# Kernel tuning notes

Measured on AMD Instinct MI355X. Metric: run time of the kernel, lower is better.

The kernel has to match this reference:

```python
import jax, jax.numpy as jnp
import numpy as np

B, S, H = 2, 2048, 2048
N_HEADS, N_KV = 16, 4
HEAD_DIM = H // N_HEADS  # 128
ROPE_THETA = 10000.0


def _rope_tables(seq_len, dim, theta):
    inv_freq = 1.0 / (theta ** (jnp.arange(0, dim, 2, dtype=jnp.float32) / dim))
    t = jnp.arange(seq_len, dtype=jnp.float32)
    freqs = jnp.outer(t, inv_freq)                 # [S, dim/2]
    emb = jnp.concatenate([freqs, freqs], axis=-1)  # [S, dim]
    return jnp.cos(emb), jnp.sin(emb)


def _rotate_half(x):
    x1, x2 = jnp.split(x, 2, axis=-1)
    return jnp.concatenate([-x2, x1], axis=-1)


def setup_inputs() -> dict:
    key = jax.random.key(0)
    ks = jax.random.split(key, 8)
    sc = 0.02
    return {
        "hidden_states": jax.random.normal(ks[0], (B, S, H), jnp.float32),
        "Wq": jax.random.normal(ks[1], (H, N_HEADS * HEAD_DIM), jnp.float32) * sc,
        "bq": jax.random.normal(ks[2], (N_HEADS * HEAD_DIM,), jnp.float32) * sc,
        "Wk": jax.random.normal(ks[3], (H, N_KV * HEAD_DIM), jnp.float32) * sc,
        "bk": jax.random.normal(ks[4], (N_KV * HEAD_DIM,), jnp.float32) * sc,
        "Wv": jax.random.normal(ks[5], (H, N_KV * HEAD_DIM), jnp.float32) * sc,
        "bv": jax.random.normal(ks[6], (N_KV * HEAD_DIM,), jnp.float32) * sc,
        "Wo": jax.random.normal(ks[7], (N_HEADS * HEAD_DIM, H), jnp.float32) * sc,
    }


def reference(hidden_states, Wq, bq, Wk, bk, Wv, bv, Wo):
    bsz, q_len, _ = hidden_states.shape
    q = hidden_states @ Wq + bq  # [B,S,nH*D]
    k = hidden_states @ Wk + bk  # [B,S,nKV*D]
    v = hidden_states @ Wv + bv
    q = q.reshape(bsz, q_len, N_HEADS, HEAD_DIM).transpose(0, 2, 1, 3)   # [B,nH,S,D]
    k = k.reshape(bsz, q_len, N_KV, HEAD_DIM).transpose(0, 2, 1, 3)      # [B,nKV,S,D]
    v = v.reshape(bsz, q_len, N_KV, HEAD_DIM).transpose(0, 2, 1, 3)

    cos, sin = _rope_tables(q_len, HEAD_DIM, ROPE_THETA)  # [S,D]
    cos = cos[None, None].astype(q.dtype)  # [1,1,S,D]
    sin = sin[None, None].astype(q.dtype)
    q = q * cos + _rotate_half(q) * sin
    k = k * cos + _rotate_half(k) * sin

    groups = N_HEADS // N_KV
    k_rep = jnp.repeat(k, groups, axis=1)  # [B,nH,S,D]
    v_rep = jnp.repeat(v, groups, axis=1)

    scale = 1.0 / np.sqrt(HEAD_DIM)
    scores = jnp.einsum("bhqd,bhkd->bhqk", q, k_rep) * scale
    attn = jax.nn.softmax(scores.astype(jnp.float32), axis=-1).astype(q.dtype)
    out = jnp.einsum("bhqk,bhkd->bhqd", attn, v_rep)
    out = out.transpose(0, 2, 1, 3).reshape(bsz, q_len, N_HEADS * HEAD_DIM)
    return out @ Wo
```

## Files before the change

kernel.cpp:

```cpp
#include <hip/hip_runtime.h>
#include <stdint.h>
#include <math.h>

typedef unsigned int u32;
typedef __bf16 bf16x8 __attribute__((ext_vector_type(8)));
typedef float  f32x4  __attribute__((ext_vector_type(4)));
typedef float  f32x16 __attribute__((ext_vector_type(16)));
typedef unsigned int u32x4 __attribute__((ext_vector_type(4)));
typedef unsigned short u16x4 __attribute__((ext_vector_type(4)));
typedef unsigned short u16x8 __attribute__((ext_vector_type(8)));

#define DEV __device__ __forceinline__

DEV unsigned short f2b(float f) {
  u32 x = __builtin_bit_cast(u32, f);
  u32 r = (x + 0x7fffu + ((x >> 16) & 1u)) >> 16;
  return (unsigned short)r;
}
DEV float b2f(unsigned short u) { return __builtin_bit_cast(float, ((u32)u) << 16); }

DEV u32 cvtpk_bf16(float lo, float hi) {
  u32 r;
  asm("v_cvt_pk_bf16_f32 %0, %1, %2" : "=v"(r) : "v"(lo), "v"(hi));
  return r;
}
DEV void pl32swap(u32& a, u32& b) {
  asm("v_permlane32_swap_b32 %0, %1" : "+v"(a), "+v"(b));
}

DEV void gl2lds16(const void* g, void* l) {
  __builtin_amdgcn_global_load_lds((const __attribute__((address_space(1))) u32*)g,
                                   (__attribute__((address_space(3))) u32*)l, 16, 0, 0);
}


__global__ void rope_tables_k(float* __restrict__ ct, float* __restrict__ st) {
  int s = blockIdx.x;
  int d = threadIdx.x;
  float inv = powf(10000.0f, -(float)d / 64.0f);
  float a = (float)s * inv;
  ct[s * 64 + d] = cosf(a);
  st[s * 64 + d] = sinf(a);
}

__global__ void packX_k(const float* __restrict__ in, unsigned short* __restrict__ out,
                        int Mtot) {
  int i = blockIdx.x * blockDim.x + threadIdx.x;
  int k8 = i & 255;
  int m = i >> 8;
  if (m >= Mtot) return;
  const float4* p = (const float4*)(in + (size_t)m * 2048 + (k8 << 3));
  float4 v0 = p[0], v1 = p[1];
  u16x8 r = { f2b(v0.x), f2b(v0.y), f2b(v0.z), f2b(v0.w),
              f2b(v1.x), f2b(v1.y), f2b(v1.z), f2b(v1.w) };
  int kt = k8 >> 2;
  int ko = (k8 & 3) << 3;
  *(u16x8*)(out + ((size_t)kt * Mtot + m) * 32 + ko) = r;
}

__global__ void packWall_k(const float* __restrict__ Wq, const float* __restrict__ Wk,
                           const float* __restrict__ Wv, const float* __restrict__ Wo,
                           unsigned short* __restrict__ Wcat,
                           unsigned short* __restrict__ Wop) {
  __shared__ float t[32][33];
  int bx = blockIdx.x;
  const float* src; unsigned short* dst; int Nd, Ncat, ncOff, nb;
  if (bx < 64)       { src = Wq; dst = Wcat; Nd = 2048; Ncat = 3072; ncOff = 0;    nb = bx; }
  else if (bx < 80)  { src = Wk; dst = Wcat; Nd = 512;  Ncat = 3072; ncOff = 2048; nb = bx - 64; }
  else if (bx < 96)  { src = Wv; dst = Wcat; Nd = 512;  Ncat = 3072; ncOff = 2560; nb = bx - 80; }
  else               { src = Wo; dst = Wop;  Nd = 2048; Ncat = 2048; ncOff = 0;    nb = bx - 96; }
  int n0 = nb << 5, k0 = blockIdx.y << 5;
  int tx = threadIdx.x, ty = threadIdx.y;
  for (int i = ty; i < 32; i += 8) t[i][tx] = src[(size_t)(k0 + i) * Nd + n0 + tx];
  __syncthreads();
  for (int i = ty; i < 32; i += 8)
    dst[((size_t)(k0 >> 5) * Ncat + ncOff + n0 + i) * 32 + tx] = f2b(t[tx][i]);
}

template <int MODE, int GX>
__global__ __launch_bounds__(256, 3) void gemm3s_k(
    const unsigned short* __restrict__ Ap, const unsigned short* __restrict__ Bp,
    float* __restrict__ outF, unsigned short* __restrict__ outQ,
    unsigned short* __restrict__ outK, unsigned short* __restrict__ outV,
    const float* __restrict__ bq_, const float* __restrict__ bk_,
    const float* __restrict__ bv_, const float* __restrict__ ctab,
    const float* __restrict__ stab, int Mtot, int Ntot) {
  constexpr int NST = 64;
  __shared__ alignas(16) char shm[49152];
  unsigned short* Al = (unsigned short*)shm;
  unsigned short* Bl = (unsigned short*)(shm + 24576);
  float* ex = (float*)shm;

  const int tid = threadIdx.x, lane = tid & 63, wid = tid >> 6;
  const int wm = wid >> 1, wn = wid & 1;
  const int cl = lane & 15, g = lane >> 4;

  const int bid = blockIdx.x;
  const int by = ((bid & 7) << 2) + ((bid >> 3) / GX);
  const int bx = (bid >> 3) % GX;
  const int row0 = by << 7, col0 = bx << 7;

  const int c0 = wid, c1 = wid + 4;
  const int sr0 = (c0 << 4) + (lane >> 2);
  const int sr1 = (c1 << 4) + (lane >> 2);
  const int sl0 = (lane & 3) ^ ((sr0 >> 1) & 3);
  const int sl1 = (lane & 3) ^ ((sr1 >> 1) & 3);
  const size_t dA = (size_t)Mtot * 32, dB = (size_t)Ntot * 32;
  const unsigned short* pa0 = Ap + (size_t)(row0 + sr0) * 32 + (sl0 << 3);
  const unsigned short* pa1 = Ap + (size_t)(row0 + sr1) * 32 + (sl1 << 3);
  const unsigned short* pb0 = Bp + (size_t)(col0 + sr0) * 32 + (sl0 << 3);
  const unsigned short* pb1 = Bp + (size_t)(col0 + sr1) * 32 + (sl1 << 3);
  const int ld0 = (c0 << 9) + (lane << 3);
  const int ld1 = (c1 << 9) + (lane << 3);

  int sslot = 0;
  auto stage = [&]() {
    const int bb = sslot << 12;
    gl2lds16(pa0, &Al[bb + ld0]);
    gl2lds16(pa1, &Al[bb + ld1]);
    gl2lds16(pb0, &Bl[bb + ld0]);
    gl2lds16(pb1, &Bl[bb + ld1]);
    pa0 += dA; pa1 += dA; pb0 += dB; pb1 += dB;
    sslot = sslot == 2 ? 0 : sslot + 1;
  };

  int aoff[4], boff[4];
#pragma unroll
  for (int m = 0; m < 4; ++m) {
    int row = (wm << 6) + (m << 4) + cl;
    aoff[m] = (row << 5) + ((g ^ ((row >> 1) & 3)) << 3);
    row = (wn << 6) + (m << 4) + cl;
    boff[m] = (row << 5) + ((g ^ ((row >> 1) & 3)) << 3);
  }

  f32x4 acc[4][4];
#pragma unroll
  for (int m = 0; m < 4; ++m)
#pragma unroll
    for (int n = 0; n < 4; ++n) acc[m][n] = (f32x4){0.f, 0.f, 0.f, 0.f};

#define STEP(RS, DO_STAGE)                                                         \
  do {                                                                             \
    const int bb_ = (RS) << 12;                                                    \
    bf16x8 af[4], bfr[4];                                                          \
    _Pragma("unroll") for (int m = 0; m < 4; ++m)                                  \
        af[m] = *(const bf16x8*)&Al[bb_ + aoff[m]];                                \
    _Pragma("unroll") for (int n = 0; n < 4; ++n)                                  \
        bfr[n] = *(const bf16x8*)&Bl[bb_ + boff[n]];                               \
    if (DO_STAGE) stage();                                                         \
    __builtin_amdgcn_s_setprio(1);                                                 \
    _Pragma("unroll") for (int m = 0; m < 4; ++m)                                  \
      _Pragma("unroll") for (int n = 0; n < 4; ++n)                                \
        acc[m][n] = __builtin_amdgcn_mfma_f32_16x16x32_bf16(af[m], bfr[n],         \
                                                            acc[m][n], 0, 0, 0);  \
    __builtin_amdgcn_s_setprio(0);                                                 \
  } while (0)

  stage(); stage();
  asm volatile("s_waitcnt vmcnt(4)" ::: "memory");
  __builtin_amdgcn_s_barrier();

  int rslot = 0;
  for (int s = 0; s < NST - 2; ++s) {
    STEP(rslot, true);
    asm volatile("s_waitcnt vmcnt(4)" ::: "memory");
    __builtin_amdgcn_s_barrier();
    rslot = rslot == 2 ? 0 : rslot + 1;
  }
  STEP(rslot, false);
  asm volatile("s_waitcnt vmcnt(0)" ::: "memory");
  __builtin_amdgcn_s_barrier();
  rslot = rslot == 2 ? 0 : rslot + 1;
  STEP(rslot, false);
#undef STEP
  __syncthreads();

  if constexpr (MODE == 0) {
#pragma unroll
    for (int mt = 0; mt < 4; ++mt) {
      int rbase = row0 + (wm << 6) + (mt << 4) + (g << 2);
#pragma unroll
      for (int nt = 0; nt < 4; ++nt) {
        int col = col0 + (wn << 6) + (nt << 4) + cl;
#pragma unroll
        for (int r = 0; r < 4; ++r)
          outF[(size_t)(rbase + r) * Ntot + col] = acc[mt][nt][r];
      }
    }
  } else {
    if (col0 >= 2560) {
#pragma unroll
      for (int mt = 0; mt < 4; ++mt) {
        int rbase = row0 + (wm << 6) + (mt << 4) + (g << 2);
#pragma unroll
        for (int nt = 0; nt < 4; ++nt) {
          int col = col0 + (wn << 6) + (nt << 4) + cl;
          int c2 = col - 2560, kk = c2 >> 7, d = c2 & 127;
          float bv2 = bv_[c2];
#pragma unroll
          for (int r = 0; r < 4; ++r) {
            int rr = rbase + r;
            int bb = rr >> 11, ss = rr & 2047;
            outV[((((size_t)bb << 2) + kk) * 128 + d) * 2048 + ss] =
                f2b(acc[mt][nt][r] + bv2);
          }
        }
      }
    } else {
      const bool isQ = col0 < 2048;
      const float* bias = isQ ? (bq_ + col0) : (bk_ + (col0 - 2048));
      if (wn == 1) {
#pragma unroll
        for (int mt = 0; mt < 4; ++mt) {
#pragma unroll
          for (int nt = 0; nt < 4; ++nt) {
            int d2 = (nt << 4) + cl;
            float b2 = bias[64 + d2];
#pragma unroll
            for (int r = 0; r < 4; ++r) {
              int lrow = (wm << 6) + (mt << 4) + (g << 2) + r;
              ex[lrow * 65 + d2] = acc[mt][nt][r] + b2;
            }
          }
        }
      }
      __syncthreads();
      if (wn == 0) {
        const int hh = isQ ? (col0 >> 7) : ((col0 - 2048) >> 7);
#pragma unroll
        for (int mt = 0; mt < 4; ++mt) {
#pragma unroll
          for (int nt = 0; nt < 4; ++nt) {
            int d = (nt << 4) + cl;
            float b1 = bias[d];
#pragma unroll
            for (int r = 0; r < 4; ++r) {
              int lrow = (wm << 6) + (mt << 4) + (g << 2) + r;
              int grow = row0 + lrow;
              int bb = grow >> 11, ss = grow & 2047;
              float x1 = acc[mt][nt][r] + b1;
              float x2 = ex[lrow * 65 + d];
              float c = ctab[ss * 64 + d], sn = stab[ss * 64 + d];
              float o1 = x1 * c - x2 * sn;
              float o2 = x2 * c + x1 * sn;
              if (isQ) { o1 *= 0.08838834764831845f; o2 *= 0.08838834764831845f; }
              unsigned short* dp = isQ
                  ? outQ + ((((size_t)bb << 4) + hh) * 2048 + ss) * 128
                  : outK + ((((size_t)bb << 2) + hh) * 2048 + ss) * 128;
              dp[d] = f2b(o1);
              dp[d + 64] = f2b(o2);
            }
          }
        }
      }
    }
  }
}

__global__ __launch_bounds__(256, 2) void attn2_k(
    const unsigned short* __restrict__ Qb, const unsigned short* __restrict__ Kb,
    const unsigned short* __restrict__ Vt, unsigned short* __restrict__ AOp) {
  __shared__ alignas(16) unsigned short Ks[2][64 * 128];
  __shared__ alignas(16) unsigned short Vs[2][128 * 64];

  const int tid = threadIdx.x, lane = tid & 63, wid = tid >> 6;
  const int hw = blockIdx.x;
  const int work = ((hw & 7) << 6) | (hw >> 3);
  const int qblk = work & 15, bh = work >> 4;
  const int b = bh >> 4, h = bh & 15, kvh = h >> 2;
  const int q0 = qblk << 7;
  const int cl = lane & 31, hi = lane >> 5;

  const unsigned short* Qp = Qb + ((size_t)(b * 16 + h) << 11) * 128;
  const unsigned short* Kp = Kb + ((size_t)(b * 4 + kvh) << 11) * 128;
  const unsigned short* Vp = Vt + ((size_t)(b * 4 + kvh) << 7) * 2048;

  const int qrow = q0 + (wid << 5) + cl;
  bf16x8 qf[8];
#pragma unroll
  for (int c = 0; c < 8; ++c)
    qf[c] = *(const bf16x8*)(Qp + (size_t)qrow * 128 + (c << 4) + (hi << 3));

  f32x16 o[4];
#pragma unroll
  for (int dt = 0; dt < 4; ++dt)
#pragma unroll
    for (int r = 0; r < 16; ++r) o[dt][r] = 0.f;
  float m = -3e38f, l = 0.f;

  auto stage = [&](int t, int buf) {
    const int kv0 = t << 6;
#pragma unroll
    for (int i = 0; i < 4; ++i) {
      int row = (wid << 4) + (i << 2) + (lane >> 4);
      int sl = (lane & 15) ^ (row & 15);
      gl2lds16(Kp + ((size_t)(kv0 + row) << 7) + (sl << 3),
               &Ks[buf][(wid << 11) + (i << 9) + (lane << 3)]);
    }
#pragma unroll
    for (int i = 0; i < 4; ++i) {
      int row = (wid << 5) + (i << 3) + (lane >> 3);
      int sl = (lane & 7) ^ (row & 7);
      gl2lds16(Vp + ((size_t)row << 11) + kv0 + (sl << 3),
               &Vs[buf][(wid << 11) + (i << 9) + (lane << 3)]);
    }
  };

  auto pack8 = [&](float a0, float a1, float a2, float a3,
                   float a4, float a5, float a6, float a7) -> u32x4 {
    u32 x0 = cvtpk_bf16(a0, a1);
    u32 y0 = cvtpk_bf16(a4, a5);
    u32 x1 = cvtpk_bf16(a2, a3);
    u32 y1 = cvtpk_bf16(a6, a7);
    pl32swap(x0, y0);
    pl32swap(x1, y1);
    return (u32x4){x0, x1, y0, y1};
  };

  stage(0, 0);
  __syncthreads();

  for (int t = 0; t < 32; ++t) {
    const int buf = t & 1;
    if (t + 1 < 32) stage(t + 1, buf ^ 1);

    f32x16 s0, s1;
#pragma unroll
    for (int r = 0; r < 16; ++r) { s0[r] = 0.f; s1[r] = 0.f; }
#pragma unroll
    for (int c = 0; c < 8; ++c) {
      int sl0 = ((c << 1) + hi) ^ (cl & 15);
      bf16x8 kf0 = *(const bf16x8*)&Ks[buf][(cl << 7) + (sl0 << 3)];
      s0 = __builtin_amdgcn_mfma_f32_32x32x16_bf16(kf0, qf[c], s0, 0, 0, 0);
    }
#pragma unroll
    for (int c = 0; c < 8; ++c) {
      int row = 32 + cl;
      int sl1 = ((c << 1) + hi) ^ (row & 15);
      bf16x8 kf1 = *(const bf16x8*)&Ks[buf][(row << 7) + (sl1 << 3)];
      s1 = __builtin_amdgcn_mfma_f32_32x32x16_bf16(kf1, qf[c], s1, 0, 0, 0);
    }

    float mx = s0[0];
#pragma unroll
    for (int r = 1; r < 16; ++r) mx = fmaxf(mx, s0[r]);
#pragma unroll
    for (int r = 0; r < 16; ++r) mx = fmaxf(mx, s1[r]);
    mx = fmaxf(mx, __shfl_xor(mx, 32));

    if (!__all(mx <= m + 8.0f)) {
      float mn = fmaxf(m, mx);
      float al = __expf(m - mn);
      m = mn;
      l *= al;
#pragma unroll
      for (int dt = 0; dt < 4; ++dt)
#pragma unroll
        for (int r = 0; r < 16; ++r) o[dt][r] *= al;
    }

    float sum = 0.f;
#pragma unroll
    for (int r = 0; r < 16; ++r) { s0[r] = __expf(s0[r] - m); sum += s0[r]; }
#pragma unroll
    for (int r = 0; r < 16; ++r) { s1[r] = __expf(s1[r] - m); sum += s1[r]; }
    l += sum;

    u32x4 w0 = pack8(s0[0], s0[1], s0[2], s0[3], s0[4], s0[5], s0[6], s0[7]);
    u32x4 w1 = pack8(s0[8], s0[9], s0[10], s0[11], s0[12], s0[13], s0[14], s0[15]);
    u32x4 w2 = pack8(s1[0], s1[1], s1[2], s1[3], s1[4], s1[5], s1[6], s1[7]);
    u32x4 w3 = pack8(s1[8], s1[9], s1[10], s1[11], s1[12], s1[13], s1[14], s1[15]);
    bf16x8 pa0 = __builtin_bit_cast(bf16x8, w0);
    bf16x8 pa1 = __builtin_bit_cast(bf16x8, w1);
    bf16x8 pa2 = __builtin_bit_cast(bf16x8, w2);
    bf16x8 pa3 = __builtin_bit_cast(bf16x8, w3);

#pragma unroll
    for (int dt = 0; dt < 4; ++dt) {
      int row = (dt << 5) + cl;
      int sb = row << 6;
      int rx = row & 7;
      bf16x8 vf0 = *(const bf16x8*)&Vs[buf][sb + (((hi) ^ rx) << 3)];
      o[dt] = __builtin_amdgcn_mfma_f32_32x32x16_bf16(vf0, pa0, o[dt], 0, 0, 0);
      bf16x8 vf1 = *(const bf16x8*)&Vs[buf][sb + (((2 + hi) ^ rx) << 3)];
      o[dt] = __builtin_amdgcn_mfma_f32_32x32x16_bf16(vf1, pa1, o[dt], 0, 0, 0);
      bf16x8 vf2 = *(const bf16x8*)&Vs[buf][sb + (((4 + hi) ^ rx) << 3)];
      o[dt] = __builtin_amdgcn_mfma_f32_32x32x16_bf16(vf2, pa2, o[dt], 0, 0, 0);
      bf16x8 vf3 = *(const bf16x8*)&Vs[buf][sb + (((6 + hi) ^ rx) << 3)];
      o[dt] = __builtin_amdgcn_mfma_f32_32x32x16_bf16(vf3, pa3, o[dt], 0, 0, 0);
    }
    __syncthreads();
  }

  float inv = 1.0f / (l + __shfl_xor(l, 32));
  const int rowi = b * 2048 + qrow;
#pragma unroll
  for (int dt = 0; dt < 4; ++dt) {
    unsigned short* base = AOp + (((size_t)((h << 2) + dt)) * 4096 + rowi) * 32;
#pragma unroll
    for (int rq = 0; rq < 4; ++rq) {
      u16x4 pk = { f2b(o[dt][(rq << 2) + 0] * inv), f2b(o[dt][(rq << 2) + 1] * inv),
                   f2b(o[dt][(rq << 2) + 2] * inv), f2b(o[dt][(rq << 2) + 3] * inv) };
      *(u16x4*)(base + (rq << 3) + (hi << 2)) = pk;
    }
  }
}

extern "C" void kernel_launch(void* const* d_in, const int* in_sizes, int n_in,
                              void* d_out, int out_size, void* d_ws, size_t ws_size,
                              hipStream_t stream) {
  const float* X  = (const float*)d_in[0];
  const float* Wq = (const float*)d_in[1];
  const float* bq = (const float*)d_in[2];
  const float* Wk = (const float*)d_in[3];
  const float* bk = (const float*)d_in[4];
  const float* Wv = (const float*)d_in[5];
  const float* bv = (const float*)d_in[6];
  const float* Wo = (const float*)d_in[7];
  float* out = (float*)d_out;

  char* ws = (char*)d_ws;
  size_t off = 0;
  auto alloc = [&](size_t bytes) {
    char* p = ws + off;
    off += (bytes + 255) & ~(size_t)255;
    return p;
  };
  unsigned short* Xp   = (unsigned short*)alloc(4096ull * 2048 * 2);
  unsigned short* Wcat = (unsigned short*)alloc(3072ull * 2048 * 2);
  unsigned short* Wop  = (unsigned short*)alloc(2048ull * 2048 * 2);
  unsigned short* Qb   = (unsigned short*)alloc(2ull * 16 * 2048 * 128 * 2);
  unsigned short* Kb   = (unsigned short*)alloc(2ull * 4 * 2048 * 128 * 2);
  unsigned short* Vt   = (unsigned short*)alloc(2ull * 4 * 128 * 2048 * 2);
  unsigned short* AOp  = (unsigned short*)alloc(4096ull * 2048 * 2);
  float* ctab = (float*)alloc(2048ull * 64 * 4);
  float* stab = (float*)alloc(2048ull * 64 * 4);

  rope_tables_k<<<dim3(2048), dim3(64), 0, stream>>>(ctab, stab);
  packX_k<<<dim3(4096), dim3(256), 0, stream>>>(X, Xp, 4096);
  packWall_k<<<dim3(160, 64), dim3(32, 8), 0, stream>>>(Wq, Wk, Wv, Wo, Wcat, Wop);

  gemm3s_k<3, 24><<<dim3(768), dim3(256), 0, stream>>>(
      Xp, Wcat, nullptr, Qb, Kb, Vt, bq, bk, bv, ctab, stab, 4096, 3072);

  attn2_k<<<dim3(512), dim3(256), 0, stream>>>(Qb, Kb, Vt, AOp);

  gemm3s_k<0, 16><<<dim3(512), dim3(256), 0, stream>>>(
      AOp, Wop, out, nullptr, nullptr, nullptr, nullptr, nullptr, nullptr,
      nullptr, nullptr, 4096, 2048);
}
```

Measured before the change: 204.8 us.

## Fold log2e into Q scale, re-swizzle V LDS layout, add MFMA priority hints

Folds log2(e) into the Q pre-scale so the softmax can use native exp2 instead of expf. V tiles are re-laid out in LDS as 64 rows by 128 columns with a 16-way XOR swizzle, which is meant to cut bank conflicts on the PV fragment reads. Global source pointers for the K and V tile loads are now computed once outside the loop. s_setprio raises wave priority around the MFMA blocks, and the row-max reduction is restructured. The exp2 rewrite slightly changes where rounding happens, and the new swizzle has to map V elements exactly right to stay correct.

```diff
diff --git a/kernel.cpp b/kernel.cpp
--- a/kernel.cpp
+++ b/kernel.cpp
@@ -243,7 +243,10 @@
               float c = ctab[ss * 64 + d], sn = stab[ss * 64 + d];
               float o1 = x1 * c - x2 * sn;
               float o2 = x2 * c + x1 * sn;
-              if (isQ) { o1 *= 0.08838834764831845f; o2 *= 0.08838834764831845f; }
+              if (isQ) {
+                o1 *= (0.08838834764831845f * 1.4426950408889634f);
+                o2 *= (0.08838834764831845f * 1.4426950408889634f);
+              }
               unsigned short* dp = isQ
                   ? outQ + ((((size_t)bb << 4) + hh) * 2048 + ss) * 128
                   : outK + ((((size_t)bb << 2) + hh) * 2048 + ss) * 128;
@@ -261,7 +264,7 @@
     const unsigned short* __restrict__ Qb, const unsigned short* __restrict__ Kb,
     const unsigned short* __restrict__ Vt, unsigned short* __restrict__ AOp) {
   __shared__ alignas(16) unsigned short Ks[2][64 * 128];
-  __shared__ alignas(16) unsigned short Vs[2][128 * 64];
+  __shared__ alignas(16) unsigned short Vs[2][64 * 128];
 
   const int tid = threadIdx.x, lane = tid & 63, wid = tid >> 6;
   const int hw = blockIdx.x;
@@ -281,30 +284,45 @@
   for (int c = 0; c < 8; ++c)
     qf[c] = *(const bf16x8*)(Qp + (size_t)qrow * 128 + (c << 4) + (hi << 3));
 
+  const unsigned short* ksrc[4];
+  int kldo[4];
+  const unsigned short* vsrc[4];
+  int vldo[4];
+#pragma unroll
+  for (int i = 0; i < 4; ++i) {
+    {
+      int row = (wid << 4) + (i << 2) + (lane >> 4);
+      int sl = (lane & 15) ^ (row & 15);
+      ksrc[i] = Kp + ((size_t)row << 7) + (sl << 3);
+      kldo[i] = (wid << 11) + (i << 9) + (lane << 3);
+    }
+    {
+      int c = (wid << 2) + i;
+      int r = (c << 2) + (lane >> 4);
+      int sp = lane & 15;
+      int slog = sp ^ (r & 15);
+      int d = (slog & 8) ? (r + 64) : r;
+      int kvo = (slog & 7) << 3;
+      vsrc[i] = Vp + (size_t)d * 2048 + kvo;
+      vldo[i] = (c << 9) + (lane << 3);
+    }
+  }
+
+  auto stage = [&](int t, int buf) {
+#pragma unroll
+    for (int i = 0; i < 4; ++i)
+      gl2lds16(ksrc[i] + ((size_t)t << 13), &Ks[buf][kldo[i]]);
+#pragma unroll
+    for (int i = 0; i < 4; ++i)
+      gl2lds16(vsrc[i] + (t << 6), &Vs[buf][vldo[i]]);
+  };
+
   f32x16 o[4];
 #pragma unroll
   for (int dt = 0; dt < 4; ++dt)
 #pragma unroll
     for (int r = 0; r < 16; ++r) o[dt][r] = 0.f;
   float m = -3e38f, l = 0.f;
-
-  auto stage = [&](int t, int buf) {
-    const int kv0 = t << 6;
-#pragma unroll
-    for (int i = 0; i < 4; ++i) {
-      int row = (wid << 4) + (i << 2) + (lane >> 4);
-      int sl = (lane & 15) ^ (row & 15);
-      gl2lds16(Kp + ((size_t)(kv0 + row) << 7) + (sl << 3),
-               &Ks[buf][(wid << 11) + (i << 9) + (lane << 3)]);
-    }
-#pragma unroll
-    for (int i = 0; i < 4; ++i) {
-      int row = (wid << 5) + (i << 3) + (lane >> 3);
-      int sl = (lane & 7) ^ (row & 7);
-      gl2lds16(Vp + ((size_t)row << 11) + kv0 + (sl << 3),
-               &Vs[buf][(wid << 11) + (i << 9) + (lane << 3)]);
-    }
-  };
 
   auto pack8 = [&](float a0, float a1, float a2, float a3,
                    float a4, float a5, float a6, float a7) -> u32x4 {
@@ -327,6 +345,7 @@
     f32x16 s0, s1;
 #pragma unroll
     for (int r = 0; r < 16; ++r) { s0[r] = 0.f; s1[r] = 0.f; }
+    __builtin_amdgcn_s_setprio(1);
 #pragma unroll
     for (int c = 0; c < 8; ++c) {
       int sl0 = ((c << 1) + hi) ^ (cl & 15);
@@ -340,17 +359,18 @@
       bf16x8 kf1 = *(const bf16x8*)&Ks[buf][(row << 7) + (sl1 << 3)];
       s1 = __builtin_amdgcn_mfma_f32_32x32x16_bf16(kf1, qf[c], s1, 0, 0, 0);
     }
-
-    float mx = s0[0];
-#pragma unroll
-    for (int r = 1; r < 16; ++r) mx = fmaxf(mx, s0[r]);
-#pragma unroll
-    for (int r = 0; r < 16; ++r) mx = fmaxf(mx, s1[r]);
+    __builtin_amdgcn_s_setprio(0);
+
+    float mx = fmaxf(s0[0], s0[1]);
+#pragma unroll
+    for (int r = 2; r < 16; r += 2) mx = fmaxf(fmaxf(mx, s0[r]), s0[r + 1]);
+#pragma unroll
+    for (int r = 0; r < 16; r += 2) mx = fmaxf(fmaxf(mx, s1[r]), s1[r + 1]);
     mx = fmaxf(mx, __shfl_xor(mx, 32));
 
     if (!__all(mx <= m + 8.0f)) {
       float mn = fmaxf(m, mx);
-      float al = __expf(m - mn);
+      float al = __builtin_amdgcn_exp2f(m - mn);
       m = mn;
       l *= al;
 #pragma unroll
@@ -361,9 +381,9 @@
 
     float sum = 0.f;
 #pragma unroll
-    for (int r = 0; r < 16; ++r) { s0[r] = __expf(s0[r] - m); sum += s0[r]; }
-#pragma unroll
-    for (int r = 0; r < 16; ++r) { s1[r] = __expf(s1[r] - m); sum += s1[r]; }
+    for (int r = 0; r < 16; ++r) { s0[r] = __builtin_amdgcn_exp2f(s0[r] - m); sum += s0[r]; }
+#pragma unroll
+    for (int r = 0; r < 16; ++r) { s1[r] = __builtin_amdgcn_exp2f(s1[r] - m); sum += s1[r]; }
     l += sum;
 
     u32x4 w0 = pack8(s0[0], s0[1], s0[2], s0[3], s0[4], s0[5], s0[6], s0[7]);
@@ -375,20 +395,24 @@
     bf16x8 pa2 = __builtin_bit_cast(bf16x8, w2);
     bf16x8 pa3 = __builtin_bit_cast(bf16x8, w3);
 
+    __builtin_amdgcn_s_setprio(1);
 #pragma unroll
     for (int dt = 0; dt < 4; ++dt) {
-      int row = (dt << 5) + cl;
-      int sb = row << 6;
-      int rx = row & 7;
-      bf16x8 vf0 = *(const bf16x8*)&Vs[buf][sb + (((hi) ^ rx) << 3)];
+      int d = (dt << 5) + cl;
+      int row = d & 63;
+      int rx = row & 15;
+      int sb = row << 7;
+      int bs = (dt & 2) << 2;
+      bf16x8 vf0 = *(const bf16x8*)&Vs[buf][sb + (((bs + 0 + hi) ^ rx) << 3)];
       o[dt] = __builtin_amdgcn_mfma_f32_32x32x16_bf16(vf0, pa0, o[dt], 0, 0, 0);
-      bf16x8 vf1 = *(const bf16x8*)&Vs[buf][sb + (((2 + hi) ^ rx) << 3)];
+      bf16x8 vf1 = *(const bf16x8*)&Vs[buf][sb + (((bs + 2 + hi) ^ rx) << 3)];
       o[dt] = __builtin_amdgcn_mfma_f32_32x32x16_bf16(vf1, pa1, o[dt], 0, 0, 0);
-      bf16x8 vf2 = *(const bf16x8*)&Vs[buf][sb + (((4 + hi) ^ rx) << 3)];
+      bf16x8 vf2 = *(const bf16x8*)&Vs[buf][sb + (((bs + 4 + hi) ^ rx) << 3)];
       o[dt] = __builtin_amdgcn_mfma_f32_32x32x16_bf16(vf2, pa2, o[dt], 0, 0, 0);
-      bf16x8 vf3 = *(const bf16x8*)&Vs[buf][sb + (((6 + hi) ^ rx) << 3)];
+      bf16x8 vf3 = *(const bf16x8*)&Vs[buf][sb + (((bs + 6 + hi) ^ rx) << 3)];
       o[dt] = __builtin_amdgcn_mfma_f32_32x32x16_bf16(vf3, pa3, o[dt], 0, 0, 0);
     }
+    __builtin_amdgcn_s_setprio(0);
     __syncthreads();
   }
 
```

Result: no change. 203.5 us (-0.7%).
